# Performance work log

Measured on AMD Instinct MI355X. Metric: run time of the kernel, lower is better.

## Reference

```python
import jax, jax.numpy as jnp
import numpy as np

N_BATCH = 4194304  # 2^22 elements -> ~200 MB per 12-bit input tensor
N_BITS = 12

# Spiking logic gates on binary {0,1} float spikes, expressed arithmetically
# (identical truth tables to the SNN XOR/AND/OR gate modules).
def _xor(a, b):
    return a + b - 2.0 * a * b

def _or(a, b):
    return a + b - a * b

def setup_inputs() -> dict:
    key = jax.random.key(0)
    kA, kB = jax.random.split(key)
    A = jax.random.bernoulli(kA, 0.5, (N_BATCH, N_BITS)).astype(jnp.float32)
    B = jax.random.bernoulli(kB, 0.5, (N_BATCH, N_BITS)).astype(jnp.float32)
    return {"A": A, "B": B}

def reference(A, B):
    """12-bit ripple-carry adder (MSB at index 0). Returns (sum [...,12], carry_out [...,1])."""
    # Reorder bits LSB-first and move bit axis to front for the carry scan.
    A_bits = jnp.moveaxis(A, -1, 0)[::-1]  # [12, N]
    B_bits = jnp.moveaxis(B, -1, 0)[::-1]
    carry0 = jnp.zeros_like(A_bits[0])

    def step(carry, ab):
        a, b = ab
        t1 = _xor(a, b)
        s = _xor(t1, carry)
        # carry_out = (a&b) | (a&c) | (b&c)
        new_carry = _or(_or(a * b, a * carry), b * carry)
        return new_carry, s

    carry, sums = jax.lax.scan(step, carry0, (A_bits, B_bits))
    sums = jnp.moveaxis(sums[::-1], 0, -1)  # back to MSB-first, [..., 12]
    return sums, carry[..., None]
```

## Files before the change

kernel.cpp:

```cpp
#include <hip/hip_runtime.h>


typedef float f32x4 __attribute__((ext_vector_type(4)));
typedef unsigned u32x4 __attribute__((ext_vector_type(4)));

struct Win { u32x4 a0, a1, a2, b0, b1, b2; };

__device__ __forceinline__ unsigned bperm(unsigned src, int srclane) {
    return (unsigned)__builtin_amdgcn_ds_bpermute(srclane << 2, (int)src);
}

__device__ __forceinline__ float bit2f(unsigned bit) {
    return __uint_as_float(0x3F800000u & (0u - bit));
}

__device__ __forceinline__ unsigned nib(u32x4 u) {
    return ((u.x >> 20) & 8u) | ((u.y >> 21) & 4u) |
           ((u.z >> 22) & 2u) | ((u.w >> 23) & 1u);
}

__global__ __launch_bounds__(256) void adder12_pf_kernel(
    const float* __restrict__ A, const float* __restrict__ B,
    float* __restrict__ sums, float* __restrict__ carry, int nrows) {
    const int lane = threadIdx.x & 63;
    const int waveRow = threadIdx.x & 192;
    const int nwin = nrows >> 8;

    auto loadw = [&](int w) {
        Win r;
        const size_t fbase = (((size_t)w << 8) + waveRow) * 12;
        const u32x4* a4 = reinterpret_cast<const u32x4*>(A + fbase) + lane;
        const u32x4* b4 = reinterpret_cast<const u32x4*>(B + fbase) + lane;
        r.a0 = a4[0]; r.a1 = a4[64]; r.a2 = a4[128];
        r.b0 = b4[0]; r.b1 = b4[64]; r.b2 = b4[128];
        return r;
    };

    Win cur = loadw(blockIdx.x);
    for (int w = blockIdx.x; w < nwin; w += gridDim.x) {
        const int wn = w + gridDim.x;
        Win nxt;
        if (wn < nwin) nxt = loadw(wn);

        const unsigned packedA = nib(cur.a0) | (nib(cur.a1) << 4) | (nib(cur.a2) << 8);
        const unsigned packedB = nib(cur.b0) | (nib(cur.b1) << 4) | (nib(cur.b2) << 8);

        unsigned ra = 0, rb = 0;
#pragma unroll
        for (int j = 0; j < 3; ++j) {
            const int q = 3 * lane + j;
            const unsigned va = bperm(packedA, q & 63);
            const unsigned vb = bperm(packedB, q & 63);
            const int sh = 4 * (q >> 6);
            ra = (ra << 4) | ((va >> sh) & 0xFu);
            rb = (rb << 4) | ((vb >> sh) & 0xFu);
        }
        const unsigned s = ra + rb;

        const size_t rowbase = ((size_t)w << 8) + waveRow;
        __builtin_nontemporal_store(bit2f(s >> 12), carry + rowbase + lane);

        f32x4* o4 = reinterpret_cast<f32x4*>(sums + rowbase * 12);
#pragma unroll
        for (int k = 0; k < 3; ++k) {
            const int p = lane + (k << 6);
            const int r = p / 3;
            const int m = p - 3 * r;
            const unsigned sv = bperm(s, r);
            const int b0 = 11 - (m << 2);
            f32x4 ov;
            ov.x = bit2f((sv >> b0) & 1u);
            ov.y = bit2f((sv >> (b0 - 1)) & 1u);
            ov.z = bit2f((sv >> (b0 - 2)) & 1u);
            ov.w = bit2f((sv >> (b0 - 3)) & 1u);
            __builtin_nontemporal_store(ov, o4 + p);
        }

        cur = nxt;
    }
}

extern "C" void kernel_launch(void* const* d_in, const int* in_sizes, int n_in,
                              void* d_out, int out_size, void* d_ws, size_t ws_size,
                              hipStream_t stream) {
    const float* A = (const float*)d_in[0];
    const float* B = (const float*)d_in[1];
    const int n = in_sizes[0] / 12;
    float* sums = (float*)d_out;
    float* carry = sums + (size_t)n * 12;

    const int block = 256;
    const int nwin = n >> 8;
    int grid = nwin < 2048 ? nwin : 2048;
    adder12_pf_kernel<<<grid, block, 0, stream>>>(A, B, sums, carry, n);
}
```

Before: 117.7 us.

## Replace persistent prefetching grid-stride loop with one block per window

Drops the persistent 2048-block grid-stride loop with software prefetch and launches one 256-thread block per 256-row window, so each thread does a single load-compute-store pass. It also switches the nontemporal stores to ordinary stores. The aim is to let the hardware scheduler hide memory latency through many resident blocks instead of explicit double-buffering, with lower register use. The cost is more block launch overhead, and the output may now pollute the cache.

```diff
diff --git a/kernel.cpp b/kernel.cpp
--- a/kernel.cpp
+++ b/kernel.cpp
@@ -3,8 +3,6 @@
 
 typedef float f32x4 __attribute__((ext_vector_type(4)));
 typedef unsigned u32x4 __attribute__((ext_vector_type(4)));
-
-struct Win { u32x4 a0, a1, a2, b0, b1, b2; };
 
 __device__ __forceinline__ unsigned bperm(unsigned src, int srclane) {
     return (unsigned)__builtin_amdgcn_ds_bpermute(srclane << 2, (int)src);
@@ -19,64 +17,50 @@
            ((u.z >> 22) & 2u) | ((u.w >> 23) & 1u);
 }
 
-__global__ __launch_bounds__(256) void adder12_pf_kernel(
+__global__ __launch_bounds__(256) void adder12_block_kernel(
     const float* __restrict__ A, const float* __restrict__ B,
-    float* __restrict__ sums, float* __restrict__ carry, int nrows) {
+    float* __restrict__ sums, float* __restrict__ carry) {
     const int lane = threadIdx.x & 63;
     const int waveRow = threadIdx.x & 192;
-    const int nwin = nrows >> 8;
 
-    auto loadw = [&](int w) {
-        Win r;
-        const size_t fbase = (((size_t)w << 8) + waveRow) * 12;
-        const u32x4* a4 = reinterpret_cast<const u32x4*>(A + fbase) + lane;
-        const u32x4* b4 = reinterpret_cast<const u32x4*>(B + fbase) + lane;
-        r.a0 = a4[0]; r.a1 = a4[64]; r.a2 = a4[128];
-        r.b0 = b4[0]; r.b1 = b4[64]; r.b2 = b4[128];
-        return r;
-    };
+    const size_t rowbase = ((size_t)blockIdx.x << 8) + waveRow;
+    const size_t fbase = rowbase * 12;
+    const u32x4* a4 = reinterpret_cast<const u32x4*>(A + fbase) + lane;
+    const u32x4* b4 = reinterpret_cast<const u32x4*>(B + fbase) + lane;
 
-    Win cur = loadw(blockIdx.x);
-    for (int w = blockIdx.x; w < nwin; w += gridDim.x) {
-        const int wn = w + gridDim.x;
-        Win nxt;
-        if (wn < nwin) nxt = loadw(wn);
+    const u32x4 ua0 = a4[0], ua1 = a4[64], ua2 = a4[128];
+    const u32x4 ub0 = b4[0], ub1 = b4[64], ub2 = b4[128];
+    const unsigned packedA = nib(ua0) | (nib(ua1) << 4) | (nib(ua2) << 8);
+    const unsigned packedB = nib(ub0) | (nib(ub1) << 4) | (nib(ub2) << 8);
 
-        const unsigned packedA = nib(cur.a0) | (nib(cur.a1) << 4) | (nib(cur.a2) << 8);
-        const unsigned packedB = nib(cur.b0) | (nib(cur.b1) << 4) | (nib(cur.b2) << 8);
+    unsigned ra = 0, rb = 0;
+#pragma unroll
+    for (int j = 0; j < 3; ++j) {
+        const int q = 3 * lane + j;
+        const unsigned va = bperm(packedA, q & 63);
+        const unsigned vb = bperm(packedB, q & 63);
+        const int sh = 4 * (q >> 6);
+        ra = (ra << 4) | ((va >> sh) & 0xFu);
+        rb = (rb << 4) | ((vb >> sh) & 0xFu);
+    }
+    const unsigned s = ra + rb;
 
-        unsigned ra = 0, rb = 0;
+    carry[rowbase + lane] = bit2f(s >> 12);
+
+    f32x4* o4 = reinterpret_cast<f32x4*>(sums + fbase);
 #pragma unroll
-        for (int j = 0; j < 3; ++j) {
-            const int q = 3 * lane + j;
-            const unsigned va = bperm(packedA, q & 63);
-            const unsigned vb = bperm(packedB, q & 63);
-            const int sh = 4 * (q >> 6);
-            ra = (ra << 4) | ((va >> sh) & 0xFu);
-            rb = (rb << 4) | ((vb >> sh) & 0xFu);
-        }
-        const unsigned s = ra + rb;
-
-        const size_t rowbase = ((size_t)w << 8) + waveRow;
-        __builtin_nontemporal_store(bit2f(s >> 12), carry + rowbase + lane);
-
-        f32x4* o4 = reinterpret_cast<f32x4*>(sums + rowbase * 12);
-#pragma unroll
-        for (int k = 0; k < 3; ++k) {
-            const int p = lane + (k << 6);
-            const int r = p / 3;
-            const int m = p - 3 * r;
-            const unsigned sv = bperm(s, r);
-            const int b0 = 11 - (m << 2);
-            f32x4 ov;
-            ov.x = bit2f((sv >> b0) & 1u);
-            ov.y = bit2f((sv >> (b0 - 1)) & 1u);
-            ov.z = bit2f((sv >> (b0 - 2)) & 1u);
-            ov.w = bit2f((sv >> (b0 - 3)) & 1u);
-            __builtin_nontemporal_store(ov, o4 + p);
-        }
-
-        cur = nxt;
+    for (int k = 0; k < 3; ++k) {
+        const int p = lane + (k << 6);
+        const int r = p / 3;
+        const int m = p - 3 * r;
+        const unsigned sv = bperm(s, r);
+        const int b0 = 11 - (m << 2);
+        f32x4 ov;
+        ov.x = bit2f((sv >> b0) & 1u);
+        ov.y = bit2f((sv >> (b0 - 1)) & 1u);
+        ov.z = bit2f((sv >> (b0 - 2)) & 1u);
+        ov.w = bit2f((sv >> (b0 - 3)) & 1u);
+        o4[p] = ov;
     }
 }
 
@@ -90,7 +74,6 @@
     float* carry = sums + (size_t)n * 12;
 
     const int block = 256;
-    const int nwin = n >> 8;
-    int grid = nwin < 2048 ? nwin : 2048;
-    adder12_pf_kernel<<<grid, block, 0, stream>>>(A, B, sums, carry, n);
+    const int grid = n >> 8;
+    adder12_block_kernel<<<grid, block, 0, stream>>>(A, B, sums, carry);
 }
```

After: 115.3 us. 2.1% less time.
